# Kernel optimization log

Hardware: AMD Instinct MI355X
Metric: run time of the kernel (lower is better)

Reference implementation:

```python
import jax, jax.numpy as jnp
import numpy as np

C = 64
CQ = C // 8


def setup_inputs() -> dict:
    key = jax.random.key(0)
    ks = jax.random.split(key, 8)
    x = jax.random.normal(ks[0], (8, C, 64, 64), dtype=jnp.float32)
    s = 1.0 / np.sqrt(C)
    Wq = jax.random.normal(ks[1], (CQ, C), dtype=jnp.float32) * s
    bq = jax.random.normal(ks[2], (CQ,), dtype=jnp.float32) * s
    Wk = jax.random.normal(ks[3], (CQ, C), dtype=jnp.float32) * s
    bk = jax.random.normal(ks[4], (CQ,), dtype=jnp.float32) * s
    Wv = jax.random.normal(ks[5], (C, C), dtype=jnp.float32) * s
    bv = jax.random.normal(ks[6], (C,), dtype=jnp.float32) * s
    gamma = jnp.array([0.5], dtype=jnp.float32)  # nonzero so value path contributes
    return {"x": x, "Wq": Wq, "bq": bq, "Wk": Wk, "bk": bk, "Wv": Wv, "bv": bv, "gamma": gamma}


def reference(x, Wq, bq, Wk, bk, Wv, bv, gamma):
    B, Cc, H, W = x.shape
    xf = x.reshape(B, Cc, H * W)  # [B, C, N]
    # 1x1 conv == channel-mixing linear
    f = jnp.einsum('oc,bcn->bon', Wq, xf) + bq[None, :, None]  # [B, C/8, N]
    g = jnp.einsum('oc,bcn->bon', Wk, xf) + bk[None, :, None]  # [B, C/8, N]
    h = jnp.einsum('oc,bcn->bon', Wv, xf) + bv[None, :, None]  # [B, C, N]
    # scores[b,i,j] = f[b,:,i] . g[b,:,j]; softmax over dim=1 (query dim i)
    scores = jnp.einsum('bdi,bdj->bij', f, g)  # [B, N, N]
    beta = jax.nn.softmax(scores, axis=1)
    o = gamma[0] * jnp.einsum('bcn,bnm->bcm', h, beta) + xf
    return o.reshape(B, Cc, H, W)
```

## Files before the change

kernel.cpp:

```cpp
#include <hip/hip_runtime.h>
#include <hip/hip_fp16.h>


typedef _Float16 half8_t __attribute__((ext_vector_type(8)));
typedef _Float16 half4_t __attribute__((ext_vector_type(4)));
typedef _Float16 half2_t __attribute__((ext_vector_type(2)));
typedef __fp16  fp16x2  __attribute__((ext_vector_type(2)));
typedef float float4_t __attribute__((ext_vector_type(4)));
typedef unsigned int uintx4 __attribute__((ext_vector_type(4)));

#define NTOK 4096
#define PRH 72
#define LOG2E 1.44269504088896340736f

#if __has_builtin(__builtin_amdgcn_exp2f)
__device__ __forceinline__ float fexp2(float x) { return __builtin_amdgcn_exp2f(x); }
#else
__device__ __forceinline__ float fexp2(float x) { return exp2f(x); }
#endif

__device__ __forceinline__ half2_t pkcvt(float a, float b) {
    fp16x2 v = __builtin_amdgcn_cvt_pkrtz(a, b);
    return __builtin_bit_cast(half2_t, v);
}

__device__ __forceinline__ float4_t mfma16(half4_t a, half4_t b, float4_t c) {
    return __builtin_amdgcn_mfma_f32_16x16x16f16(a, b, c, 0, 0, 0);
}
__device__ __forceinline__ float4_t mfma32(half8_t a, half8_t b, float4_t c) {
    return __builtin_amdgcn_mfma_f32_16x16x32_f16(a, b, c, 0, 0, 0);
}

#define GLDS(G, L) __builtin_amdgcn_global_load_lds(                            \
    (const __attribute__((address_space(1))) unsigned int*)(G),                 \
    (__attribute__((address_space(3))) unsigned int*)(L), 16, 0, 0)

#define WAITVM4_BAR() do {                                                      \
    __builtin_amdgcn_sched_barrier(0);                                          \
    asm volatile("s_waitcnt vmcnt(4)" ::: "memory");                            \
    __builtin_amdgcn_sched_barrier(0);                                          \
    __builtin_amdgcn_s_barrier();                                               \
} while (0)

__global__ __launch_bounds__(320) void proj_kernel(
    const float* __restrict__ x,
    const float* __restrict__ Wq, const float* __restrict__ bq,
    const float* __restrict__ Wk, const float* __restrict__ bk,
    const float* __restrict__ Wv, const float* __restrict__ bv,
    __half* __restrict__ fTR, __half* __restrict__ gT16, __half* __restrict__ hM)
{
    __shared__ __align__(16) _Float16 xh[32 * PRH];
    const int t      = threadIdx.x;
    const int blk    = blockIdx.x;
    const int b      = blockIdx.y;
    const int n0     = blk * 32;
    const int kt64   = blk >> 1;
    const int t4base = (blk & 1) * 2;

    if (t < 256) {
#pragma unroll
        for (int i = 0; i < 2; i++) {
            const int idx = t + i * 256;
            const int c = idx >> 3, f4 = idx & 7;
            float4 v = *(const float4*)(x + (((size_t)(b * 64 + c)) << 12) + n0 + f4 * 4);
            const int cs = c ^ ((f4 & 3) << 4);
            xh[(f4 * 4 + 0) * PRH + cs] = (_Float16)v.x;
            xh[(f4 * 4 + 1) * PRH + cs] = (_Float16)v.y;
            xh[(f4 * 4 + 2) * PRH + cs] = (_Float16)v.z;
            xh[(f4 * 4 + 3) * PRH + cs] = (_Float16)v.w;
        }
    }

    const int w    = t >> 6;
    const int lane = t & 63;
    const int q    = lane >> 4;
    const int ml   = lane & 15;

    const float* wrow;
    if (w == 0) wrow = (ml < 8) ? (Wq + ml * 64) : (Wk + (ml - 8) * 64);
    else        wrow = Wv + ((w - 1) * 16 + ml) * 64;
    half4_t afr[4];
#pragma unroll
    for (int ks = 0; ks < 4; ks++) {
        float4 wv4 = *(const float4*)(wrow + ks * 16 + q * 4);
        afr[ks] = (half4_t){(_Float16)wv4.x, (_Float16)wv4.y,
                            (_Float16)wv4.z, (_Float16)wv4.w};
    }
    float4 bias4;
    if (w == 0) bias4 = (q < 2) ? *(const float4*)(bq + q * 4)
                                : *(const float4*)(bk + (q - 2) * 4);
    else        bias4 = *(const float4*)(bv + (w - 1) * 16 + q * 4);

    __syncthreads();

    float4_t acc2[2];
#pragma unroll
    for (int cg = 0; cg < 2; cg++) {
        const int tok  = cg * 16 + ml;
        const int swz  = (tok >> 2) & 3;
        float4_t acc = (float4_t){0.f, 0.f, 0.f, 0.f};
#pragma unroll
        for (int ks = 0; ks < 4; ks++) {
            half4_t bfr = *(const half4_t*)(&xh[tok * PRH + ((ks ^ swz) * 16 + q * 4)]);
            acc = __builtin_amdgcn_mfma_f32_16x16x16f16(afr[ks], bfr, acc, 0, 0, 0);
        }
        acc[0] += bias4.x; acc[1] += bias4.y; acc[2] += bias4.z; acc[3] += bias4.w;
        acc2[cg] = acc;
        const int gtok = n0 + tok;
        const int t4   = t4base + cg;

        if (w == 0) {
            __half* rec = fTR + ((size_t)b << 16) + (size_t)(kt64 * 16 + ml) * 64;
            if (q < 2) {
                half4_t fv = {(_Float16)(acc[0] * LOG2E), (_Float16)(acc[1] * LOG2E),
                              (_Float16)(acc[2] * LOG2E), (_Float16)(acc[3] * LOG2E)};
                *(half4_t*)(rec + q * 16 + t4 * 4) = fv;
            } else {
                half4_t cv = (half4_t){};
                if (q == 2) cv[0] = (_Float16)1.0f;
                *(half4_t*)(rec + q * 16 + t4 * 4) = cv;
            }
            float gn2p = acc[0] * acc[0] + acc[1] * acc[1] +
                         acc[2] * acc[2] + acc[3] * acc[3];
            float gn2 = gn2p + __shfl_xor(gn2p, 16, 64);
            if (q >= 2) {
                half4_t gv = {(_Float16)acc[0], (_Float16)acc[1],
                              (_Float16)acc[2], (_Float16)acc[3]};
                __half* gp = gT16 + (size_t)((b << 12) + gtok) * 16;
                *(half4_t*)(gp + (q - 2) * 4) = gv;
                if (q == 2) {
                    const float M = (LOG2E * 4.6f) * __builtin_sqrtf(gn2) + 1.0f;
                    *(half4_t*)(gp + 8) = (half4_t){(_Float16)(-M), 0, 0, 0};
                } else {
                    *(half4_t*)(gp + 12) = (half4_t){};
                }
            }
        }
    }

    __syncthreads();
    if (w > 0) {
        const int ch = (w - 1) * 16 + q * 4;
#pragma unroll
        for (int cg = 0; cg < 2; cg++) {
            const int loc = ((ml >> 2) << 3) + (cg << 2) + (ml & 3);
#pragma unroll
            for (int r = 0; r < 4; r++)
                xh[(ch + r) * 36 + loc] = (_Float16)acc2[cg][r];
        }
    }
    __syncthreads();
    if (t < 256) {
        const int ch   = t >> 2;
        const int part = t & 3;
        half8_t v = *(const half8_t*)(&xh[ch * 36 + part * 8]);
        __half* dst = hM + ((size_t)(b * 64 + ch) << 12) + (size_t)kt64 * 64
                         + (blk & 1) * 32 + part * 8;
        *(half8_t*)dst = v;
    }
}


#define LDAH(V0, V1, V2, V3, HP)                                                \
    half8_t V0 = *(const half8_t*)(HP);                                         \
    half8_t V1 = *(const half8_t*)((HP) + 1024);                                \
    half8_t V2 = *(const half8_t*)((HP) + 2048);                                \
    half8_t V3 = *(const half8_t*)((HP) + 3072);

#define QK(F, N)                                                                \
    float4_t N##A0, N##B0, N##A1, N##B1;                                        \
    {                                                                           \
        half4_t a0 = __builtin_shufflevector(F, F, 0, 1, 2, 3);                 \
        half4_t a1 = __builtin_shufflevector(F, F, 4, 5, 6, 7);                 \
        __builtin_amdgcn_s_setprio(1);                                          \
        N##A0 = mfma16(a0, gfA, z4);                                            \
        N##B0 = mfma16(a0, gfB, z4);                                            \
        N##A1 = mfma16(a1, gfA, z4);                                            \
        N##B1 = mfma16(a1, gfB, z4);                                            \
        __builtin_amdgcn_s_setprio(0);                                          \
    }

#define PAIRC(N, H0, H1, H2, H3)                                                \
    {                                                                           \
        float eA0 = fexp2(N##A0[0]), eA1 = fexp2(N##A0[1]),                     \
              eA2 = fexp2(N##A0[2]), eA3 = fexp2(N##A0[3]);                     \
        float oA0 = fexp2(N##A1[0]), oA1 = fexp2(N##A1[1]),                     \
              oA2 = fexp2(N##A1[2]), oA3 = fexp2(N##A1[3]);                     \
        float eB0 = fexp2(N##B0[0]), eB1 = fexp2(N##B0[1]),                     \
              eB2 = fexp2(N##B0[2]), eB3 = fexp2(N##B0[3]);                     \
        float oB0 = fexp2(N##B1[0]), oB1 = fexp2(N##B1[1]),                     \
              oB2 = fexp2(N##B1[2]), oB3 = fexp2(N##B1[3]);                     \
        uintx4 puA = {__builtin_bit_cast(unsigned int, pkcvt(eA0, eA1)),        \
                      __builtin_bit_cast(unsigned int, pkcvt(eA2, eA3)),        \
                      __builtin_bit_cast(unsigned int, pkcvt(oA0, oA1)),        \
                      __builtin_bit_cast(unsigned int, pkcvt(oA2, oA3))};       \
        uintx4 puB = {__builtin_bit_cast(unsigned int, pkcvt(eB0, eB1)),        \
                      __builtin_bit_cast(unsigned int, pkcvt(eB2, eB3)),        \
                      __builtin_bit_cast(unsigned int, pkcvt(oB0, oB1)),        \
                      __builtin_bit_cast(unsigned int, pkcvt(oB2, oB3))};       \
        half8_t pA8 = __builtin_bit_cast(half8_t, puA);                         \
        half8_t pB8 = __builtin_bit_cast(half8_t, puB);                         \
        __builtin_amdgcn_s_setprio(1);                                          \
        accLA = mfma32(ones8, pA8, accLA);                                      \
        accLB = mfma32(ones8, pB8, accLB);                                      \
        accA[0] = mfma32(H0, pA8, accA[0]); accB[0] = mfma32(H0, pB8, accB[0]); \
        accA[1] = mfma32(H1, pA8, accA[1]); accB[1] = mfma32(H1, pB8, accB[1]); \
        accA[2] = mfma32(H2, pA8, accA[2]); accB[2] = mfma32(H2, pB8, accB[2]); \
        accA[3] = mfma32(H3, pA8, accA[3]); accB[3] = mfma32(H3, pB8, accB[3]); \
        __builtin_amdgcn_s_setprio(0);                                          \
    }

template<int NT>
__global__ __launch_bounds__(256) void attn_kernel(
    const __half* __restrict__ fTR, const __half* __restrict__ gT16,
    const __half* __restrict__ hM,
    __half* __restrict__ Pacc, float* __restrict__ Lsum)
{
    __shared__ __align__(16) _Float16 hl[2][8192];
    const int tid   = threadIdx.x;
    const int w     = tid >> 6;
    const int lane  = tid & 63;
    const int q     = lane >> 4;
    const int ml    = lane & 15;
    const int m7    = ml & 7;
    const int b     = blockIdx.y;
    const int split = blockIdx.z;
    const int colA  = blockIdx.x * 128 + w * 16 + ml;
    const int colB  = colA + 64;

    half4_t gfA = *(const half4_t*)(gT16 + ((size_t)((b << 12) + colA)) * 16 + q * 4);
    half4_t gfB = *(const half4_t*)(gT16 + ((size_t)((b << 12) + colB)) * 16 + q * 4);

    float4_t accA[4], accB[4];
#pragma unroll
    for (int cg = 0; cg < 4; cg++) {
        accA[cg] = (float4_t){0.f, 0.f, 0.f, 0.f};
        accB[cg] = (float4_t){0.f, 0.f, 0.f, 0.f};
    }
    float4_t accLA = (float4_t){0.f, 0.f, 0.f, 0.f};
    float4_t accLB = (float4_t){0.f, 0.f, 0.f, 0.f};
    const half8_t ones8 = {(_Float16)1.0f, (_Float16)1.0f, (_Float16)1.0f,
                           (_Float16)1.0f, (_Float16)1.0f, (_Float16)1.0f,
                           (_Float16)1.0f, (_Float16)1.0f};
    const float4_t z4 = (float4_t){0.f, 0.f, 0.f, 0.f};

    const int k64 = split * NT * 2;

    const int ch0  = tid >> 3;
    const int gsw  = (tid & 7) ^ (ch0 & 7);
    const __half* hs0 = hM + ((size_t)(b * 64 + ch0) << 12) + (size_t)k64 * 64 + gsw * 8;
    const __half* hs1 = hs0 + ((size_t)32 << 12);
    const __half* fptr = fTR + ((size_t)b << 16) + (size_t)(k64 * 16 + ml) * 64 + q * 16;

    const int gxa = ((q ^ m7) << 3);
    const int gxb = (((4 + q) ^ m7) << 3);

    GLDS(hs0,      &hl[0][tid * 8]);
    GLDS(hs1,      &hl[0][2048 + tid * 8]);
    GLDS(hs0 + 64, &hl[0][4096 + tid * 8]);
    GLDS(hs1 + 64, &hl[0][6144 + tid * 8]);
    half8_t f01 = *(const half8_t*)fptr;
    half8_t f23 = *(const half8_t*)(fptr + 8);
    half8_t f45 = *(const half8_t*)(fptr + 1024);
    half8_t f67 = *(const half8_t*)(fptr + 1032);
    __syncthreads();

    const __half* hn0 = hs0 + 128;
    const __half* hn1 = hs1 + 128;

#pragma unroll 1
    for (int kt = 0; kt < NT; kt++) {
        const _Float16* hbA = &hl[kt & 1][ml << 6];
        const _Float16* hbB = hbA + 4096;

        LDAH(a00, a01, a02, a03, hbA + gxa)
        QK(f01, s)

        if (kt + 1 < NT) {
            _Float16* nb = &hl[(kt + 1) & 1][0];
            GLDS(hn0,      nb + tid * 8);
            GLDS(hn1,      nb + 2048 + tid * 8);
            GLDS(hn0 + 64, nb + 4096 + tid * 8);
            GLDS(hn1 + 64, nb + 6144 + tid * 8);
            hn0 += 128;
            hn1 += 128;
        }

        LDAH(a10, a11, a12, a13, hbA + gxb)
        QK(f23, t)

        PAIRC(s, a00, a01, a02, a03)

        LDAH(a20, a21, a22, a23, hbB + gxa)

        PAIRC(t, a10, a11, a12, a13)

        QK(f45, u)
        LDAH(a30, a31, a32, a33, hbB + gxb)

        PAIRC(u, a20, a21, a22, a23)

        QK(f67, v)
        if (kt + 1 < NT) {
            f01 = *(const half8_t*)(fptr + 2048);
            f23 = *(const half8_t*)(fptr + 2056);
            f45 = *(const half8_t*)(fptr + 3072);
            f67 = *(const half8_t*)(fptr + 3080);
            fptr += 2048;
        }

        PAIRC(v, a30, a31, a32, a33)

        if (kt + 1 < NT) {
            WAITVM4_BAR();
        }
    }

    __half* pa = Pacc + (((size_t)(split * 8 + b) * 64) << 12);
#pragma unroll
    for (int cg = 0; cg < 4; cg++)
#pragma unroll
        for (int r = 0; r < 4; r++) {
            int ch = cg * 16 + q * 4 + r;
            pa[((size_t)ch << 12) + colA] = __float2half(accA[cg][r]);
            pa[((size_t)ch << 12) + colB] = __float2half(accB[cg][r]);
        }
    if (q == 0) {
        Lsum[((size_t)(split * 8 + b) << 12) + colA] = accLA[0];
        Lsum[((size_t)(split * 8 + b) << 12) + colB] = accLB[0];
    }
}

template<int S>
__global__ __launch_bounds__(256) void merge_kernel(
    const __half* __restrict__ Pacc, const float* __restrict__ Lsum,
    const float* __restrict__ x, const float* __restrict__ gammap,
    float* __restrict__ out)
{
    __shared__ float invL[64];
    const int tid  = threadIdx.x;
    const int c4   = tid & 15;
    const int chh  = tid >> 4;
    const int b    = blockIdx.y;
    const int col0 = blockIdx.x * 64;
    const int ch   = blockIdx.z * 16 + chh;

    if (tid < 64) {
        float L = 0.f;
#pragma unroll
        for (int s = 0; s < S; s++)
            L += Lsum[((size_t)(s * 8 + b) << 12) + col0 + tid];
        invL[tid] = gammap[0] / L;
    }
    __syncthreads();

    const int cc = c4 * 4;
    const size_t base = (((size_t)b * 64 + ch) << 12) + col0 + cc;
    float4 xv = *(const float4*)(x + base);
    float o0 = 0.f, o1 = 0.f, o2 = 0.f, o3 = 0.f;
#pragma unroll
    for (int s = 0; s < S; s++) {
        half4_t pv = *(const half4_t*)(Pacc +
            (((size_t)(s * 8 + b) * 64 + ch) << 12) + col0 + cc);
        o0 += (float)pv[0];
        o1 += (float)pv[1];
        o2 += (float)pv[2];
        o3 += (float)pv[3];
    }
    float4 ov;
    ov.x = o0 * invL[cc]     + xv.x;
    ov.y = o1 * invL[cc + 1] + xv.y;
    ov.z = o2 * invL[cc + 2] + xv.z;
    ov.w = o3 * invL[cc + 3] + xv.w;
    *(float4*)(out + base) = ov;
}

extern "C" void kernel_launch(void* const* d_in, const int* in_sizes, int n_in,
                              void* d_out, int out_size, void* d_ws, size_t ws_size,
                              hipStream_t stream) {
    const float* x     = (const float*)d_in[0];
    const float* Wq    = (const float*)d_in[1];
    const float* bq    = (const float*)d_in[2];
    const float* Wk    = (const float*)d_in[3];
    const float* bk    = (const float*)d_in[4];
    const float* Wv    = (const float*)d_in[5];
    const float* bv    = (const float*)d_in[6];
    const float* gamma = (const float*)d_in[7];
    float* out = (float*)d_out;

    const size_t fr_bytes  = (size_t)8 * 65536 * 2;
    const size_t g_bytes   = (size_t)8 * NTOK * 16 * 2;
    const size_t hM_bytes  = (size_t)8 * 64 * NTOK * 2;
    const size_t pa_split  = (size_t)8 * 64 * NTOK * 2;
    const size_t l_split   = (size_t)8 * NTOK * sizeof(float);
    const size_t base_need = fr_bytes + g_bytes + hM_bytes;

    int S = 1;
    if (ws_size >= base_need + 2 * (pa_split + l_split)) S = 2;

    char* p = (char*)d_ws;
    __half* fTR  = (__half*)p;  p += fr_bytes;
    __half* gT16 = (__half*)p;  p += g_bytes;
    __half* hM   = (__half*)p;  p += hM_bytes;
    __half* Pacc = (__half*)p;  p += (size_t)S * pa_split;
    float*  Lsum = (float*)p;

    proj_kernel<<<dim3(128, 8), 320, 0, stream>>>(x, Wq, bq, Wk, bk, Wv, bv,
                                                  fTR, gT16, hM);
    if (S == 2) {
        attn_kernel<16><<<dim3(32, 8, 2), 256, 0, stream>>>(fTR, gT16, hM, Pacc, Lsum);
        merge_kernel<2><<<dim3(64, 8, 4), 256, 0, stream>>>(Pacc, Lsum, x, gamma, out);
    } else {
        attn_kernel<32><<<dim3(32, 8, 1), 256, 0, stream>>>(fTR, gT16, hM, Pacc, Lsum);
        merge_kernel<1><<<dim3(64, 8, 4), 256, 0, stream>>>(Pacc, Lsum, x, gamma, out);
    }
}
```

Baseline: 114.5 us.

## Fuse split-K merge into attention kernel via last-block atomic counter

Removes the separate merge kernel. Each attention block writes its partial result, then bumps an atomic counter per (column tile, batch). The last of the two splits reads the other split's partial, normalizes by the summed softmax denominator, adds the residual and writes the output. In the single-split path the block writes the final output directly. This saves one launch and one full pass over the partial buffers. In exchange it adds fences, a counter reset inside the projection kernel, and a serialized tail in the last block.

```diff
diff --git a/kernel.cpp b/kernel.cpp
--- a/kernel.cpp
+++ b/kernel.cpp
@@ -47,7 +47,8 @@
     const float* __restrict__ Wq, const float* __restrict__ bq,
     const float* __restrict__ Wk, const float* __restrict__ bk,
     const float* __restrict__ Wv, const float* __restrict__ bv,
-    __half* __restrict__ fTR, __half* __restrict__ gT16, __half* __restrict__ hM)
+    __half* __restrict__ fTR, __half* __restrict__ gT16, __half* __restrict__ hM,
+    int* __restrict__ cnt)
 {
     __shared__ __align__(16) _Float16 xh[32 * PRH];
     const int t      = threadIdx.x;
@@ -56,6 +57,8 @@
     const int n0     = blk * 32;
     const int kt64   = blk >> 1;
     const int t4base = (blk & 1) * 2;
+
+    if (blk == 0 && b == 0 && t < 256) cnt[t] = 0;
 
     if (t < 256) {
 #pragma unroll
@@ -210,11 +213,13 @@
         __builtin_amdgcn_s_setprio(0);                                          \
     }
 
-template<int NT>
+template<int NT, int S>
 __global__ __launch_bounds__(256) void attn_kernel(
     const __half* __restrict__ fTR, const __half* __restrict__ gT16,
     const __half* __restrict__ hM,
-    __half* __restrict__ Pacc, float* __restrict__ Lsum)
+    __half* __restrict__ Pacc, float* __restrict__ Lsum, int* __restrict__ cnt,
+    const float* __restrict__ x, const float* __restrict__ gammap,
+    float* __restrict__ out)
 {
     __shared__ __align__(16) _Float16 hl[2][8192];
     const int tid   = threadIdx.x;
@@ -316,6 +321,24 @@
         }
     }
 
+    const float gamma = gammap[0];
+
+    if constexpr (S == 1) {
+        const float sA = gamma / accLA[0];
+        const float sB = gamma / accLB[0];
+#pragma unroll
+        for (int cg = 0; cg < 4; cg++)
+#pragma unroll
+            for (int r = 0; r < 4; r++) {
+                const int ch = cg * 16 + q * 4 + r;
+                const size_t o1 = ((size_t)(b * 64 + ch) << 12) + colA;
+                const size_t o2 = o1 + 64;
+                out[o1] = accA[cg][r] * sA + x[o1];
+                out[o2] = accB[cg][r] * sB + x[o2];
+            }
+        return;
+    }
+
     __half* pa = Pacc + (((size_t)(split * 8 + b) * 64) << 12);
 #pragma unroll
     for (int cg = 0; cg < 4; cg++)
@@ -329,50 +352,34 @@
         Lsum[((size_t)(split * 8 + b) << 12) + colA] = accLA[0];
         Lsum[((size_t)(split * 8 + b) << 12) + colB] = accLB[0];
     }
-}
-
-template<int S>
-__global__ __launch_bounds__(256) void merge_kernel(
-    const __half* __restrict__ Pacc, const float* __restrict__ Lsum,
-    const float* __restrict__ x, const float* __restrict__ gammap,
-    float* __restrict__ out)
-{
-    __shared__ float invL[64];
-    const int tid  = threadIdx.x;
-    const int c4   = tid & 15;
-    const int chh  = tid >> 4;
-    const int b    = blockIdx.y;
-    const int col0 = blockIdx.x * 64;
-    const int ch   = blockIdx.z * 16 + chh;
-
-    if (tid < 64) {
-        float L = 0.f;
-#pragma unroll
-        for (int s = 0; s < S; s++)
-            L += Lsum[((size_t)(s * 8 + b) << 12) + col0 + tid];
-        invL[tid] = gammap[0] / L;
-    }
-    __syncthreads();
-
-    const int cc = c4 * 4;
-    const size_t base = (((size_t)b * 64 + ch) << 12) + col0 + cc;
-    float4 xv = *(const float4*)(x + base);
-    float o0 = 0.f, o1 = 0.f, o2 = 0.f, o3 = 0.f;
-#pragma unroll
-    for (int s = 0; s < S; s++) {
-        half4_t pv = *(const half4_t*)(Pacc +
-            (((size_t)(s * 8 + b) * 64 + ch) << 12) + col0 + cc);
-        o0 += (float)pv[0];
-        o1 += (float)pv[1];
-        o2 += (float)pv[2];
-        o3 += (float)pv[3];
-    }
-    float4 ov;
-    ov.x = o0 * invL[cc]     + xv.x;
-    ov.y = o1 * invL[cc + 1] + xv.y;
-    ov.z = o2 * invL[cc + 2] + xv.z;
-    ov.w = o3 * invL[cc + 3] + xv.w;
-    *(float4*)(out + base) = ov;
+
+    __threadfence();
+    __syncthreads();
+    __shared__ int lastf;
+    if (tid == 0)
+        lastf = (atomicAdd(cnt + ((blockIdx.x << 3) | b), 1) == S - 1);
+    __syncthreads();
+    if (!lastf) return;
+    __threadfence();
+
+    const int os = 1 - split;
+    const __half* pb = Pacc + (((size_t)(os * 8 + b) * 64) << 12);
+    const float lA = accLA[0] + Lsum[((size_t)(os * 8 + b) << 12) + colA];
+    const float lB = accLB[0] + Lsum[((size_t)(os * 8 + b) << 12) + colB];
+    const float sA = gamma / lA;
+    const float sB = gamma / lB;
+#pragma unroll
+    for (int cg = 0; cg < 4; cg++)
+#pragma unroll
+        for (int r = 0; r < 4; r++) {
+            const int ch = cg * 16 + q * 4 + r;
+            const size_t o1 = ((size_t)(b * 64 + ch) << 12) + colA;
+            const size_t o2 = o1 + 64;
+            const float vA = accA[cg][r] + __half2float(pb[((size_t)ch << 12) + colA]);
+            const float vB = accB[cg][r] + __half2float(pb[((size_t)ch << 12) + colB]);
+            out[o1] = vA * sA + x[o1];
+            out[o2] = vB * sB + x[o2];
+        }
 }
 
 extern "C" void kernel_launch(void* const* d_in, const int* in_sizes, int n_in,
@@ -393,25 +400,27 @@
     const size_t hM_bytes  = (size_t)8 * 64 * NTOK * 2;
     const size_t pa_split  = (size_t)8 * 64 * NTOK * 2;
     const size_t l_split   = (size_t)8 * NTOK * sizeof(float);
+    const size_t cnt_bytes = 1024;
     const size_t base_need = fr_bytes + g_bytes + hM_bytes;
 
     int S = 1;
-    if (ws_size >= base_need + 2 * (pa_split + l_split)) S = 2;
+    if (ws_size >= base_need + 2 * (pa_split + l_split) + cnt_bytes) S = 2;
 
     char* p = (char*)d_ws;
     __half* fTR  = (__half*)p;  p += fr_bytes;
     __half* gT16 = (__half*)p;  p += g_bytes;
     __half* hM   = (__half*)p;  p += hM_bytes;
-    __half* Pacc = (__half*)p;  p += (size_t)S * pa_split;
-    float*  Lsum = (float*)p;
+    __half* Pacc = (__half*)p;  p += (size_t)2 * pa_split;
+    float*  Lsum = (float*)p;   p += (size_t)2 * l_split;
+    int*    cnt  = (int*)p;
 
     proj_kernel<<<dim3(128, 8), 320, 0, stream>>>(x, Wq, bq, Wk, bk, Wv, bv,
-                                                  fTR, gT16, hM);
+                                                  fTR, gT16, hM, cnt);
     if (S == 2) {
-        attn_kernel<16><<<dim3(32, 8, 2), 256, 0, stream>>>(fTR, gT16, hM, Pacc, Lsum);
-        merge_kernel<2><<<dim3(64, 8, 4), 256, 0, stream>>>(Pacc, Lsum, x, gamma, out);
+        attn_kernel<16, 2><<<dim3(32, 8, 2), 256, 0, stream>>>(
+            fTR, gT16, hM, Pacc, Lsum, cnt, x, gamma, out);
     } else {
-        attn_kernel<32><<<dim3(32, 8, 1), 256, 0, stream>>>(fTR, gT16, hM, Pacc, Lsum);
-        merge_kernel<1><<<dim3(64, 8, 4), 256, 0, stream>>>(Pacc, Lsum, x, gamma, out);
-    }
-}
+        attn_kernel<32, 1><<<dim3(32, 8, 1), 256, 0, stream>>>(
+            fTR, gT16, hM, Pacc, Lsum, cnt, x, gamma, out);
+    }
+}
```

After: 199.1 us. 73.9% more time.
